# Kernel optimization log

Hardware: AMD Instinct MI355X
Metric: run time of the kernel (lower is better)

The kernel has to match this reference:

```python
import jax, jax.numpy as jnp
import numpy as np

DIM = 2048
N_HEADS = 16
HEAD_DIM = DIM // N_HEADS  # 128
HIDDEN = 8192
EPS = 1e-6
NEG = -1e9


def rmsnorm(x, w):
    xf = x.astype(jnp.float32)
    y = xf * jax.lax.rsqrt(jnp.mean(xf * xf, axis=-1, keepdims=True) + EPS)
    return y.astype(x.dtype) * w


def apply_rope(x, cos, sin):
    # x: [B,S,H,Hd]; cos/sin: [S,Hd//2] -> broadcast [1,S,1,Hd//2]
    xf = x.astype(jnp.float32)
    xr = xf[..., 0::2]
    xi = xf[..., 1::2]
    c = cos[None, :, None, :]
    s = sin[None, :, None, :]
    or_ = xr * c - xi * s
    oi_ = xr * s + xi * c
    out = jnp.stack([or_, oi_], axis=-1).reshape(x.shape)
    return out.astype(x.dtype)


def setup_inputs() -> dict:
    key = jax.random.key(0)
    ks = jax.random.split(key, 10)
    B, S = 1, 2048
    x = jax.random.normal(ks[0], (B, S, DIM), dtype=jnp.float32)
    # RoPE frequencies (Llama-style, theta=10000)
    inv_freq = 1.0 / (10000.0 ** (jnp.arange(0, HEAD_DIM, 2, dtype=jnp.float32) / HEAD_DIM))
    angles = jnp.arange(S, dtype=jnp.float32)[:, None] * inv_freq[None, :]  # [S, Hd//2]
    freqs_cos = jnp.cos(angles)
    freqs_sin = jnp.sin(angles)
    # causal additive mask [1,1,S,S]
    mask = jnp.where(jnp.tril(jnp.ones((S, S), dtype=bool)), 0.0, NEG).astype(jnp.float32)[None, None]
    sc = 0.02
    wq = jax.random.normal(ks[1], (DIM, DIM), dtype=jnp.float32) * sc
    wk = jax.random.normal(ks[2], (DIM, DIM), dtype=jnp.float32) * sc
    wv = jax.random.normal(ks[3], (DIM, DIM), dtype=jnp.float32) * sc
    wo = jax.random.normal(ks[4], (DIM, DIM), dtype=jnp.float32) * sc
    w1 = jax.random.normal(ks[5], (DIM, HIDDEN), dtype=jnp.float32) * sc
    w2 = jax.random.normal(ks[6], (HIDDEN, DIM), dtype=jnp.float32) * sc
    w3 = jax.random.normal(ks[7], (DIM, HIDDEN), dtype=jnp.float32) * sc
    attn_norm_w = jnp.ones((DIM,), dtype=jnp.float32)
    ffn_norm_w = jnp.ones((DIM,), dtype=jnp.float32)
    return {"x": x, "freqs_cos": freqs_cos, "freqs_sin": freqs_sin, "mask": mask,
            "wq": wq, "wk": wk, "wv": wv, "wo": wo, "w1": w1, "w2": w2, "w3": w3,
            "attn_norm_w": attn_norm_w, "ffn_norm_w": ffn_norm_w}


def reference(x, freqs_cos, freqs_sin, mask, wq, wk, wv, wo, w1, w2, w3, attn_norm_w, ffn_norm_w):
    B, S, D = x.shape
    # --- attention (pre-norm) ---
    hn = rmsnorm(x, attn_norm_w)
    q = (hn @ wq).reshape(B, S, N_HEADS, HEAD_DIM)
    k = (hn @ wk).reshape(B, S, N_HEADS, HEAD_DIM)
    v = (hn @ wv).reshape(B, S, N_HEADS, HEAD_DIM)
    q = apply_rope(q, freqs_cos, freqs_sin)
    k = apply_rope(k, freqs_cos, freqs_sin)
    scores = jnp.einsum('bqhd,bkhd->bhqk', q, k) / (HEAD_DIM ** 0.5) + mask
    attn = jax.nn.softmax(scores.astype(jnp.float32), axis=-1).astype(q.dtype)
    ctx = jnp.einsum('bhqk,bkhd->bqhd', attn, v).reshape(B, S, D)
    h = x + ctx @ wo
    # --- SwiGLU FFN (pre-norm) ---
    fn = rmsnorm(h, ffn_norm_w)
    ff = (jax.nn.silu(fn @ w1) * (fn @ w3)) @ w2
    return h + ff
```

## Files before the change

kernel.cpp:

```cpp
#include <hip/hip_runtime.h>
#include <hip/hip_bf16.h>

#define DIM 2048
#define HEAD_DIM 128
#define N_HEADS 16
#define SEQ 2048
#define HID 8192
#define SQKV 6144

typedef short bf16x8 __attribute__((ext_vector_type(8)));
typedef float f32x4 __attribute__((ext_vector_type(4)));
using bf16 = __hip_bfloat16;

#define MFMA16(a, b, c) __builtin_amdgcn_mfma_f32_16x16x32_bf16(a, b, c, 0, 0, 0)

__device__ __forceinline__ unsigned short f2bu(float f) {
    union { bf16 b; unsigned short u; } cv;
    cv.b = __float2bfloat16(f);
    return cv.u;
}

__device__ __forceinline__ void gl16(const void* g, void* l) {
    __builtin_amdgcn_global_load_lds(
        (const __attribute__((address_space(1))) unsigned int*)g,
        (__attribute__((address_space(3))) unsigned int*)l, 16, 0, 0);
}

__global__ __launch_bounds__(256) void rmsnorm_bf16_k(
    const float* __restrict__ x, const float* __restrict__ w, bf16* __restrict__ y)
{
    const int row = blockIdx.x;
    const int tid = threadIdx.x;
    const float* xr = x + (size_t)row * DIM;
    float4 v0 = ((const float4*)xr)[tid];
    float4 v1 = ((const float4*)xr)[tid + 256];
    float ss = v0.x*v0.x + v0.y*v0.y + v0.z*v0.z + v0.w*v0.w
             + v1.x*v1.x + v1.y*v1.y + v1.z*v1.z + v1.w*v1.w;
    for (int o = 32; o > 0; o >>= 1) ss += __shfl_down(ss, o);
    __shared__ float red[4];
    if ((tid & 63) == 0) red[tid >> 6] = ss;
    __syncthreads();
    float tot = red[0] + red[1] + red[2] + red[3];
    float r = rsqrtf(tot * (1.0f / DIM) + 1e-6f);
    float4 w0 = ((const float4*)w)[tid];
    float4 w1 = ((const float4*)w)[tid + 256];
    ushort4 o0, o1;
    o0.x = f2bu(v0.x * r * w0.x); o0.y = f2bu(v0.y * r * w0.y);
    o0.z = f2bu(v0.z * r * w0.z); o0.w = f2bu(v0.w * r * w0.w);
    o1.x = f2bu(v1.x * r * w1.x); o1.y = f2bu(v1.y * r * w1.y);
    o1.z = f2bu(v1.z * r * w1.z); o1.w = f2bu(v1.w * r * w1.w);
    ushort4* yr = (ushort4*)(y + (size_t)row * DIM);
    yr[tid] = o0;
    yr[tid + 256] = o1;
}

__global__ __launch_bounds__(256) void rmsnorm4_k(
    const float* __restrict__ part, const float* __restrict__ x,
    const float* __restrict__ w, float* __restrict__ hout, bf16* __restrict__ y)
{
    const int row = blockIdx.x;
    const int tid = threadIdx.x;
    const size_t base = (size_t)row * DIM;
    const size_t SP = (size_t)SEQ * DIM;
    float4 r0, r1;
    float ss = 0.0f;
    {
        float4 a  = ((const float4*)(x + base))[tid];
        float4 p0 = ((const float4*)(part + base))[tid];
        float4 p1 = ((const float4*)(part + SP + base))[tid];
        float4 p2 = ((const float4*)(part + 2 * SP + base))[tid];
        float4 p3 = ((const float4*)(part + 3 * SP + base))[tid];
        r0.x = a.x + ((p0.x + p1.x) + (p2.x + p3.x));
        r0.y = a.y + ((p0.y + p1.y) + (p2.y + p3.y));
        r0.z = a.z + ((p0.z + p1.z) + (p2.z + p3.z));
        r0.w = a.w + ((p0.w + p1.w) + (p2.w + p3.w));
        ((float4*)(hout + base))[tid] = r0;
        ss += r0.x*r0.x + r0.y*r0.y + r0.z*r0.z + r0.w*r0.w;
    }
    {
        const int t2 = tid + 256;
        float4 a  = ((const float4*)(x + base))[t2];
        float4 p0 = ((const float4*)(part + base))[t2];
        float4 p1 = ((const float4*)(part + SP + base))[t2];
        float4 p2 = ((const float4*)(part + 2 * SP + base))[t2];
        float4 p3 = ((const float4*)(part + 3 * SP + base))[t2];
        r1.x = a.x + ((p0.x + p1.x) + (p2.x + p3.x));
        r1.y = a.y + ((p0.y + p1.y) + (p2.y + p3.y));
        r1.z = a.z + ((p0.z + p1.z) + (p2.z + p3.z));
        r1.w = a.w + ((p0.w + p1.w) + (p2.w + p3.w));
        ((float4*)(hout + base))[t2] = r1;
        ss += r1.x*r1.x + r1.y*r1.y + r1.z*r1.z + r1.w*r1.w;
    }
    for (int o = 32; o > 0; o >>= 1) ss += __shfl_down(ss, o);
    __shared__ float red[4];
    if ((tid & 63) == 0) red[tid >> 6] = ss;
    __syncthreads();
    float tot = red[0] + red[1] + red[2] + red[3];
    float r = rsqrtf(tot * (1.0f / DIM) + 1e-6f);
    float4 w0 = ((const float4*)w)[tid];
    float4 w1 = ((const float4*)w)[tid + 256];
    ushort4 o0, o1;
    o0.x = f2bu(r0.x * r * w0.x); o0.y = f2bu(r0.y * r * w0.y);
    o0.z = f2bu(r0.z * r * w0.z); o0.w = f2bu(r0.w * r * w0.w);
    o1.x = f2bu(r1.x * r * w1.x); o1.y = f2bu(r1.y * r * w1.y);
    o1.z = f2bu(r1.z * r * w1.z); o1.w = f2bu(r1.w * r * w1.w);
    ushort4* yr = (ushort4*)(y + base);
    yr[tid] = o0;
    yr[tid + 256] = o1;
}

__global__ __launch_bounds__(256) void reduce4_k(
    const float* __restrict__ part, const float* __restrict__ h, float* __restrict__ out)
{
    const size_t i = (size_t)blockIdx.x * 256 + threadIdx.x;
    const size_t SP4 = (size_t)SEQ * DIM / 4;
    float4 a  = ((const float4*)h)[i];
    float4 p0 = ((const float4*)part)[i];
    float4 p1 = ((const float4*)part)[i + SP4];
    float4 p2 = ((const float4*)part)[i + 2 * SP4];
    float4 p3 = ((const float4*)part)[i + 3 * SP4];
    float4 r;
    r.x = a.x + ((p0.x + p1.x) + (p2.x + p3.x));
    r.y = a.y + ((p0.y + p1.y) + (p2.y + p3.y));
    r.z = a.z + ((p0.z + p1.z) + (p2.z + p3.z));
    r.w = a.w + ((p0.w + p1.w) + (p2.w + p3.w));
    ((float4*)out)[i] = r;
}

__global__ __launch_bounds__(256) void convT_f32_bf16_k(
    const float* __restrict__ in, bf16* __restrict__ out, int R, int C)
{
    __shared__ float t[32][33];
    const int tx = threadIdx.x, ty = threadIdx.y;
    const int x0 = blockIdx.x * 32, y0 = blockIdx.y * 32;
#pragma unroll
    for (int i = 0; i < 4; ++i)
        t[ty + i * 8][tx] = in[(size_t)(y0 + ty + i * 8) * C + x0 + tx];
    __syncthreads();
#pragma unroll
    for (int i = 0; i < 4; ++i)
        out[(size_t)(x0 + ty + i * 8) * R + y0 + tx] = __float2bfloat16(t[tx][ty + i * 8]);
}

__global__ __launch_bounds__(256) void convT3_f32_bf16_k(
    const float* __restrict__ wq, const float* __restrict__ wk,
    const float* __restrict__ wv, bf16* __restrict__ out)
{
    const int z = blockIdx.z;
    const float* in = z == 0 ? wq : (z == 1 ? wk : wv);
    bf16* o = out + (size_t)z * DIM * DIM;
    __shared__ float t[32][33];
    const int tx = threadIdx.x, ty = threadIdx.y;
    const int x0 = blockIdx.x * 32, y0 = blockIdx.y * 32;
#pragma unroll
    for (int i = 0; i < 4; ++i)
        t[ty + i * 8][tx] = in[(size_t)(y0 + ty + i * 8) * DIM + x0 + tx];
    __syncthreads();
#pragma unroll
    for (int i = 0; i < 4; ++i)
        o[(size_t)(x0 + ty + i * 8) * DIM + y0 + tx] = __float2bfloat16(t[tx][ty + i * 8]);
}

__global__ __launch_bounds__(256) void transpose_bf16_k(
    const bf16* __restrict__ in, int istride, bf16* __restrict__ out)
{
    __shared__ unsigned short t[32][33];
    const int tx = threadIdx.x, ty = threadIdx.y;
    const int x = blockIdx.x * 32 + tx;
    const int y0 = blockIdx.y * 32;
    const unsigned short* inu = (const unsigned short*)in;
    unsigned short* outu = (unsigned short*)out;
#pragma unroll
    for (int i = 0; i < 4; ++i)
        t[ty + i * 8][tx] = inu[(size_t)(y0 + ty + i * 8) * istride + x];
    __syncthreads();
    const int x2 = blockIdx.y * 32 + tx;
    const int y2 = blockIdx.x * 32;
#pragma unroll
    for (int i = 0; i < 4; ++i)
        outu[(size_t)(y2 + ty + i * 8) * SEQ + x2] = t[tx][ty + i * 8];
}

__global__ __launch_bounds__(256) void rope_qk_k(
    bf16* __restrict__ q, bf16* __restrict__ k,
    const float* __restrict__ cosb, const float* __restrict__ sinb)
{
    const int gid = blockIdx.x * 256 + threadIdx.x;
    const int s = gid >> 10;
    const int p = gid & 1023;
    const int h = p >> 6, j = p & 63;
    const size_t off = (size_t)s * SQKV + h * HEAD_DIM + 2 * j;
    const float c = cosb[s * 64 + j], sn = sinb[s * 64 + j];
    float xr = __bfloat162float(q[off]), xi = __bfloat162float(q[off + 1]);
    q[off]     = __float2bfloat16(xr * c - xi * sn);
    q[off + 1] = __float2bfloat16(xr * sn + xi * c);
    xr = __bfloat162float(k[off]); xi = __bfloat162float(k[off + 1]);
    k[off]     = __float2bfloat16(xr * c - xi * sn);
    k[off + 1] = __float2bfloat16(xr * sn + xi * c);
}

template <int EP>
__global__ __launch_bounds__(512, 1) void gemm256_k(
    const bf16* __restrict__ A, const bf16* __restrict__ Bt,
    bf16* __restrict__ Cb, const bf16* other, float* __restrict__ Pf,
    int M, int N, int K, int gx, int ntile, int Ks)
{
    extern __shared__ char smem[];
    const int t512 = threadIdx.x;
    const int w = t512 >> 6, lane = t512 & 63;
    const int lr = lane & 15, lg = lane >> 4;
    const int wm = w >> 2, wn = w & 3;
    const int bofs = (wn & 1) * 64;
    const int swz = (lr & 7) << 4;

    const int nwg = gridDim.x;
    const int q8 = nwg >> 3, r8 = nwg & 7;
    const int xcd = blockIdx.x & 7, seqq = blockIdx.x >> 3;
    const int wgid = (xcd < r8 ? xcd * (q8 + 1) : r8 * (q8 + 1) + (xcd - r8) * q8) + seqq;
    const int split = wgid / ntile;
    const int tile = wgid % ntile;
    const int grp = tile / (4 * gx), rem = tile % (4 * gx);
    const int m0 = (grp * 4 + (rem & 3)) * 256, n0 = (rem >> 2) * 256;
    const int kb0 = split * Ks;
    const int niter = Ks >> 7;

    const bf16* aS[2][2]; const bf16* bS[2][2];
    int sOff[2];
#pragma unroll
    for (int c = 0; c < 2; ++c) {
        const int s = (c * 512 + t512) * 16;
        const int pp = s ^ (((s >> 7) & 7) << 4);
        const int row = pp >> 7, colE = (pp & 127) >> 1;
        sOff[c] = s;
#pragma unroll
        for (int hs = 0; hs < 2; ++hs) {
            aS[hs][c] = A  + (size_t)(m0 + hs * 128 + row) * K + kb0 + colE;
            bS[hs][c] = Bt + (size_t)(n0 + hs * 128 + row) * K + kb0 + colE;
        }
    }
    auto stA = [&](int buf, int kt, int hs) {
        char* base = smem + (buf * 2 + hs) * 16384;
        gl16(aS[hs][0] + (kt << 6), base + sOff[0]);
        gl16(aS[hs][1] + (kt << 6), base + sOff[1]);
    };
    auto stB = [&](int buf, int kt, int hs) {
        char* base = smem + 65536 + (buf * 2 + hs) * 16384;
        gl16(bS[hs][0] + (kt << 6), base + sOff[0]);
        gl16(bS[hs][1] + (kt << 6), base + sOff[1]);
    };

    const char* A0m = smem + (0 * 2 + wm) * 16384;
    const char* A1m = smem + (1 * 2 + wm) * 16384;
    const char* B0m = smem + 65536 + (0 * 2 + (wn >> 1)) * 16384;
    const char* B1m = smem + 65536 + (1 * 2 + (wn >> 1)) * 16384;

    f32x4 acc[8][4] = {};
    bf16x8 bfr[4][2];
    bf16x8 x0, x1, x2, x3;

#define SBAR __builtin_amdgcn_s_barrier()
#define LGKM0 do { asm volatile("s_waitcnt lgkmcnt(0)" ::: "memory"); \
                   __builtin_amdgcn_sched_barrier(0); } while (0)
#define WVM(n) do { asm volatile("s_waitcnt vmcnt(" #n ")" ::: "memory"); \
                    __builtin_amdgcn_sched_barrier(0); } while (0)
#define LDA4(base, mf0) do { \
    x0 = *(const bf16x8*)((base) + (((mf0) * 16 + lr) * 128) + ((lg * 16) ^ swz)); \
    x1 = *(const bf16x8*)((base) + (((mf0) * 16 + lr) * 128) + ((64 + lg * 16) ^ swz)); \
    x2 = *(const bf16x8*)((base) + ((((mf0) + 1) * 16 + lr) * 128) + ((lg * 16) ^ swz)); \
    x3 = *(const bf16x8*)((base) + ((((mf0) + 1) * 16 + lr) * 128) + ((64 + lg * 16) ^ swz)); \
    } while (0)
#define LDB8(base) do { \
    _Pragma("unroll") \
    for (int nf = 0; nf < 4; ++nf) { \
        bfr[nf][0] = *(const bf16x8*)((base) + ((bofs + nf * 16 + lr) * 128) + ((lg * 16) ^ swz)); \
        bfr[nf][1] = *(const bf16x8*)((base) + ((bofs + nf * 16 + lr) * 128) + ((64 + lg * 16) ^ swz)); \
    } } while (0)
#define MFMA_PH(mf0) do { \
    _Pragma("unroll") \
    for (int nf = 0; nf < 4; ++nf) { \
        acc[(mf0)][nf]     = MFMA16(x0, bfr[nf][0], acc[(mf0)][nf]); \
        acc[(mf0)][nf]     = MFMA16(x1, bfr[nf][1], acc[(mf0)][nf]); \
        acc[(mf0) + 1][nf] = MFMA16(x2, bfr[nf][0], acc[(mf0) + 1][nf]); \
        acc[(mf0) + 1][nf] = MFMA16(x3, bfr[nf][1], acc[(mf0) + 1][nf]); \
    } } while (0)

    stB(0, 0, 0); stB(0, 0, 1); stA(0, 0, 0); stA(0, 0, 1);
    stB(1, 1, 0); stB(1, 1, 1);
    WVM(4);
    SBAR;

    for (int t = 0; t < niter; ++t) {
        const bool pf = (t + 1 < niter);
        const int k1 = 2 * t + 1, k2 = 2 * t + 2, k3 = 2 * t + 3;

        LDB8(B0m);
        LDA4(A0m, 0);
        stA(1, k1, 0);
        SBAR; LGKM0; MFMA_PH(0); SBAR;
        LDA4(A0m, 2);
        stA(1, k1, 1);
        SBAR; LGKM0; MFMA_PH(2); SBAR;
        LDA4(A0m, 4);
        if (pf) stB(0, k2, 0);
        SBAR; LGKM0; MFMA_PH(4); SBAR;
        if (pf) { WVM(2); } else { WVM(0); }
        LDA4(A0m, 6);
        if (pf) stB(0, k2, 1);
        SBAR; LGKM0; MFMA_PH(6); SBAR;
        LDB8(B1m);
        LDA4(A1m, 0);
        if (pf) stA(0, k2, 0);
        SBAR; LGKM0; MFMA_PH(0); SBAR;
        LDA4(A1m, 2);
        if (pf) stA(0, k2, 1);
        SBAR; LGKM0; MFMA_PH(2); SBAR;
        LDA4(A1m, 4);
        if (pf) stB(1, k3, 0);
        SBAR; LGKM0; MFMA_PH(4); SBAR;
        if (pf) WVM(2);
        LDA4(A1m, 6);
        if (pf) stB(1, k3, 1);
        SBAR; LGKM0; MFMA_PH(6); SBAR;
    }
#undef SBAR
#undef LGKM0
#undef WVM
#undef LDA4
#undef LDB8
#undef MFMA_PH

    float* pf_base = Pf + (size_t)split * M * N;
#pragma unroll
    for (int mf = 0; mf < 8; ++mf)
#pragma unroll
        for (int nf = 0; nf < 4; ++nf) {
            const int row = m0 + wm * 128 + mf * 16 + lg * 4;
            const int col = n0 + wn * 64 + nf * 16 + lr;
#pragma unroll
            for (int r = 0; r < 4; ++r) {
                const size_t idx = (size_t)(row + r) * N + col;
                const float v = acc[mf][nf][r];
                if (EP == 0) {
                    Cb[idx] = __float2bfloat16(v);
                } else if (EP == 2) {
                    const float gg = __bfloat162float(other[idx]);
                    const float sg = gg / (1.0f + __expf(-gg));
                    Cb[idx] = __float2bfloat16(sg * v);
                } else {
                    pf_base[idx] = v;
                }
            }
        }
}

__global__ __launch_bounds__(256) void attn_fwd_k(
    const bf16* __restrict__ qkv, const bf16* __restrict__ vT, bf16* __restrict__ ctx)
{
    const int tid = threadIdx.x;
    const int w = tid >> 6, lane = tid & 63;
    const int lr = lane & 15, lg = lane >> 4;
    const int h = blockIdx.y;
    const int qidx = (blockIdx.y < 8) ? blockIdx.x : (31 - blockIdx.x);
    const int q0b = qidx * 64;
    const int nt = qidx + 1;

    __shared__ __align__(16) unsigned short Kt[2][64 * 128];
    __shared__ __align__(16) unsigned short Vt[2][128 * 64];
    __shared__ __align__(16) unsigned short Pp[4][16 * 64];

    const char* kbase = (const char*)(qkv + DIM + h * HEAD_DIM);
    const char* vbase = (const char*)(vT + (size_t)h * HEAD_DIM * SEQ);

    const int krow_c = tid >> 4;
    const int kcolB  = (tid & 15) * 16;
    const int vrow_c = tid >> 3;
    const int vcolB  = (tid & 7) * 16;

    auto stage = [&](int buf, int kb) {
#pragma unroll
        for (int c = 0; c < 4; ++c) {
            const int r = c * 16 + krow_c;
            gl16(kbase + (size_t)(kb + r) * (SQKV * 2) + (kcolB ^ ((r & 7) << 4)),
                 &Kt[buf][c * 2048 + tid * 8]);
        }
#pragma unroll
        for (int c = 0; c < 4; ++c) {
            const int r = c * 32 + vrow_c;
            gl16(vbase + (size_t)r * (SEQ * 2) + kb * 2 + (vcolB ^ ((r & 7) << 4)),
                 &Vt[buf][c * 2048 + tid * 8]);
        }
    };

    bf16x8 qf[4];
    const bf16* qrow = qkv + (size_t)(q0b + w * 16 + lr) * SQKV + h * HEAD_DIM;
#pragma unroll
    for (int dt = 0; dt < 4; ++dt)
        qf[dt] = *(const bf16x8*)(qrow + dt * 32 + lg * 8);

    f32x4 o[8] = {};
    float m[4], l[4];
#pragma unroll
    for (int j = 0; j < 4; ++j) { m[j] = -3e38f; l[j] = 0.0f; }
    const float scale = 0.08838834764831845f;

    stage(0, 0);
    __syncthreads();

    int cur = 0;
    for (int t = 0; t < nt; ++t) {
        const int kb = t * 64;
        if (t + 1 < nt) stage(cur ^ 1, kb + 64);

        f32x4 s[4] = {};
        __builtin_amdgcn_s_setprio(1);
#pragma unroll
        for (int ss = 0; ss < 4; ++ss) {
            const int r = ss * 16 + lr;
            const int sw = (r & 7) << 3;
#pragma unroll
            for (int dt = 0; dt < 4; ++dt) {
                bf16x8 kf = *(const bf16x8*)&Kt[cur][r * 128 + ((dt * 32 + lg * 8) ^ sw)];
                s[ss] = MFMA16(qf[dt], kf, s[ss]);
            }
        }
        __builtin_amdgcn_s_setprio(0);

        float al[4];
#pragma unroll
        for (int j = 0; j < 4; ++j) {
            const int qi = q0b + w * 16 + lg * 4 + j;
            const int prow = lg * 4 + j;
            const int psw = (prow & 7) << 3;
            float a[4];
#pragma unroll
            for (int ss = 0; ss < 4; ++ss)
                a[ss] = s[ss][j] * scale + ((kb + ss * 16 + lr) > qi ? -1e9f : 0.0f);
            float mx = fmaxf(fmaxf(a[0], a[1]), fmaxf(a[2], a[3]));
            mx = fmaxf(mx, __shfl_xor(mx, 1));
            mx = fmaxf(mx, __shfl_xor(mx, 2));
            mx = fmaxf(mx, __shfl_xor(mx, 4));
            mx = fmaxf(mx, __shfl_xor(mx, 8));
            const float mn = fmaxf(m[j], mx);
            const float asc = __expf(m[j] - mn);
            float e0 = __expf(a[0] - mn), e1 = __expf(a[1] - mn);
            float e2 = __expf(a[2] - mn), e3 = __expf(a[3] - mn);
            float rs = (e0 + e1) + (e2 + e3);
            rs += __shfl_xor(rs, 1); rs += __shfl_xor(rs, 2);
            rs += __shfl_xor(rs, 4); rs += __shfl_xor(rs, 8);
            l[j] = l[j] * asc + rs;
            m[j] = mn;
            al[j] = asc;
            Pp[w][prow * 64 + ((lr)      ^ psw)] = f2bu(e0);
            Pp[w][prow * 64 + ((16 + lr) ^ psw)] = f2bu(e1);
            Pp[w][prow * 64 + ((32 + lr) ^ psw)] = f2bu(e2);
            Pp[w][prow * 64 + ((48 + lr) ^ psw)] = f2bu(e3);
        }
#pragma unroll
        for (int d2 = 0; d2 < 8; ++d2)
#pragma unroll
            for (int j = 0; j < 4; ++j) o[d2][j] *= al[j];

        asm volatile("s_waitcnt lgkmcnt(0)" ::: "memory");
        __builtin_amdgcn_sched_barrier(0);
        const int asw = (lr & 7) << 3;
        bf16x8 pa0 = *(const bf16x8*)&Pp[w][lr * 64 + ((lg * 8)      ^ asw)];
        bf16x8 pa1 = *(const bf16x8*)&Pp[w][lr * 64 + ((32 + lg * 8) ^ asw)];

        __builtin_amdgcn_s_setprio(1);
#pragma unroll
        for (int d2 = 0; d2 < 8; ++d2) {
            const int rv = d2 * 16 + lr;
            const int vsw = (rv & 7) << 3;
            bf16x8 vf0 = *(const bf16x8*)&Vt[cur][rv * 64 + ((lg * 8)      ^ vsw)];
            bf16x8 vf1 = *(const bf16x8*)&Vt[cur][rv * 64 + ((32 + lg * 8) ^ vsw)];
            o[d2] = MFMA16(pa0, vf0, o[d2]);
            o[d2] = MFMA16(pa1, vf1, o[d2]);
        }
        __builtin_amdgcn_s_setprio(0);

        __syncthreads();
        cur ^= 1;
    }

#pragma unroll
    for (int j = 0; j < 4; ++j) {
        const float inv = 1.0f / l[j];
        bf16* dst = ctx + (size_t)(q0b + w * 16 + lg * 4 + j) * DIM + h * HEAD_DIM + lr;
#pragma unroll
        for (int d2 = 0; d2 < 8; ++d2)
            dst[d2 * 16] = __float2bfloat16(o[d2][j] * inv);
    }
}

extern "C" void kernel_launch(void* const* d_in, const int* in_sizes, int n_in,
                              void* d_out, int out_size, void* d_ws, size_t ws_size,
                              hipStream_t stream)
{
    const float* x   = (const float*)d_in[0];
    const float* fc  = (const float*)d_in[1];
    const float* fs  = (const float*)d_in[2];
    const float* wq  = (const float*)d_in[4];
    const float* wk  = (const float*)d_in[5];
    const float* wv  = (const float*)d_in[6];
    const float* wo  = (const float*)d_in[7];
    const float* w1  = (const float*)d_in[8];
    const float* w2  = (const float*)d_in[9];
    const float* w3  = (const float*)d_in[10];
    const float* anw = (const float*)d_in[11];
    const float* fnw = (const float*)d_in[12];
    float* out = (float*)d_out;

    char* p = (char*)d_ws;
    auto alloc = [&](size_t n) { char* r = p; p += (n + 255) & ~(size_t)255; return r; };
    bf16* wT  = (bf16*)alloc((size_t)HID * DIM * 2);
    bf16* hn  = (bf16*)alloc((size_t)SEQ * DIM * 2);
    bf16* qkv = (bf16*)alloc((size_t)SEQ * SQKV * 2);
    bf16* vt  = (bf16*)alloc((size_t)SEQ * DIM * 2);
    bf16* ctx = (bf16*)alloc((size_t)SEQ * DIM * 2);
    bf16* fn  = (bf16*)alloc((size_t)SEQ * DIM * 2);
    float* h  = (float*)alloc((size_t)SEQ * DIM * 4);
    bf16* g   = (bf16*)alloc((size_t)SEQ * HID * 2);
    float* sk = (float*)alloc((size_t)4 * SEQ * DIM * 4);

    const dim3 tb32(32, 8);
    const int LDS256 = 131072;
    (void)hipFuncSetAttribute((const void*)gemm256_k<0>,
        hipFuncAttributeMaxDynamicSharedMemorySize, LDS256);
    (void)hipFuncSetAttribute((const void*)gemm256_k<2>,
        hipFuncAttributeMaxDynamicSharedMemorySize, LDS256);
    (void)hipFuncSetAttribute((const void*)gemm256_k<3>,
        hipFuncAttributeMaxDynamicSharedMemorySize, LDS256);

    rmsnorm_bf16_k<<<SEQ, 256, 0, stream>>>(x, anw, hn);

    convT3_f32_bf16_k<<<dim3(DIM / 32, DIM / 32, 3), tb32, 0, stream>>>(wq, wk, wv, wT);
    gemm256_k<0><<<(SEQ / 256) * (SQKV / 256), 512, LDS256, stream>>>(
        hn, wT, qkv, nullptr, nullptr, SEQ, SQKV, DIM, SQKV / 256, (SEQ / 256) * (SQKV / 256), DIM);

    rope_qk_k<<<(SEQ * 1024) / 256, 256, 0, stream>>>(qkv, qkv + DIM, fc, fs);
    transpose_bf16_k<<<dim3(DIM / 32, SEQ / 32), tb32, 0, stream>>>(qkv + 2 * DIM, SQKV, vt);

    attn_fwd_k<<<dim3(SEQ / 64, N_HEADS), 256, 0, stream>>>(qkv, vt, ctx);

    convT_f32_bf16_k<<<dim3(DIM / 32, DIM / 32), tb32, 0, stream>>>(wo, wT, DIM, DIM);
    gemm256_k<3><<<(SEQ / 256) * (DIM / 256) * 4, 512, LDS256, stream>>>(
        ctx, wT, nullptr, nullptr, sk, SEQ, DIM, DIM, DIM / 256, (SEQ / 256) * (DIM / 256), 512);
    rmsnorm4_k<<<SEQ, 256, 0, stream>>>(sk, x, fnw, h, fn);

    convT_f32_bf16_k<<<dim3(HID / 32, DIM / 32), tb32, 0, stream>>>(w1, wT, DIM, HID);
    gemm256_k<0><<<(SEQ / 256) * (HID / 256), 512, LDS256, stream>>>(
        fn, wT, g, nullptr, nullptr, SEQ, HID, DIM, HID / 256, (SEQ / 256) * (HID / 256), DIM);
    convT_f32_bf16_k<<<dim3(HID / 32, DIM / 32), tb32, 0, stream>>>(w3, wT, DIM, HID);
    gemm256_k<2><<<(SEQ / 256) * (HID / 256), 512, LDS256, stream>>>(
        fn, wT, g, g, nullptr, SEQ, HID, DIM, HID / 256, (SEQ / 256) * (HID / 256), DIM);

    convT_f32_bf16_k<<<dim3(DIM / 32, HID / 32), tb32, 0, stream>>>(w2, wT, HID, DIM);
    gemm256_k<3><<<(SEQ / 256) * (DIM / 256) * 4, 512, LDS256, stream>>>(
        g, wT, nullptr, nullptr, sk, SEQ, DIM, HID, DIM / 256, (SEQ / 256) * (DIM / 256), 2048);
    reduce4_k<<<(SEQ * DIM / 4) / 256, 256, 0, stream>>>(sk, h, out);
}
```

Before: 510.3 us.

## Fuse w1 and w3 FFN GEMMs with interleaved weights and in-epilogue SwiGLU

The separate w1 and w3 GEMMs are replaced by one GEMM over a combined B matrix of 2*HID columns. B rows are interleaved in 16-row groups from the w1 and w3 transposes, so each wave holds matching gate and up accumulators and computes silu(a)*b in the epilogue. This removes the intermediate write and re-read of the gate tensor and one kernel launch. The w3 transpose reuses the dead hn/qkv workspace region. MFMA phases are also wrapped in s_setprio to favour the math waves during scheduling.

```diff
diff --git a/kernel.cpp b/kernel.cpp
--- a/kernel.cpp
+++ b/kernel.cpp
@@ -201,8 +201,8 @@
 
 template <int EP>
 __global__ __launch_bounds__(512, 1) void gemm256_k(
-    const bf16* __restrict__ A, const bf16* __restrict__ Bt,
-    bf16* __restrict__ Cb, const bf16* other, float* __restrict__ Pf,
+    const bf16* __restrict__ A, const bf16* __restrict__ Bt, const bf16* __restrict__ Bt2,
+    bf16* __restrict__ Cb, float* __restrict__ Pf,
     int M, int N, int K, int gx, int ntile, int Ks)
 {
     extern __shared__ char smem[];
@@ -234,8 +234,16 @@
         sOff[c] = s;
 #pragma unroll
         for (int hs = 0; hs < 2; ++hs) {
-            aS[hs][c] = A  + (size_t)(m0 + hs * 128 + row) * K + kb0 + colE;
-            bS[hs][c] = Bt + (size_t)(n0 + hs * 128 + row) * K + kb0 + colE;
+            aS[hs][c] = A + (size_t)(m0 + hs * 128 + row) * K + kb0 + colE;
+            const int rg = n0 + hs * 128 + row;
+            if (EP == 4) {
+                const int g = rg >> 4;
+                const bf16* src = (g & 1) ? Bt2 : Bt;
+                const int j = ((g >> 1) << 4) + (rg & 15);
+                bS[hs][c] = src + (size_t)j * K + kb0 + colE;
+            } else {
+                bS[hs][c] = Bt + (size_t)rg * K + kb0 + colE;
+            }
         }
     }
     auto stA = [&](int buf, int kt, int hs) {
@@ -276,13 +284,15 @@
         bfr[nf][1] = *(const bf16x8*)((base) + ((bofs + nf * 16 + lr) * 128) + ((64 + lg * 16) ^ swz)); \
     } } while (0)
 #define MFMA_PH(mf0) do { \
+    __builtin_amdgcn_s_setprio(1); \
     _Pragma("unroll") \
     for (int nf = 0; nf < 4; ++nf) { \
         acc[(mf0)][nf]     = MFMA16(x0, bfr[nf][0], acc[(mf0)][nf]); \
         acc[(mf0)][nf]     = MFMA16(x1, bfr[nf][1], acc[(mf0)][nf]); \
         acc[(mf0) + 1][nf] = MFMA16(x2, bfr[nf][0], acc[(mf0) + 1][nf]); \
         acc[(mf0) + 1][nf] = MFMA16(x3, bfr[nf][1], acc[(mf0) + 1][nf]); \
-    } } while (0)
+    } \
+    __builtin_amdgcn_s_setprio(0); } while (0)
 
     stB(0, 0, 0); stB(0, 0, 1); stA(0, 0, 0); stA(0, 0, 1);
     stB(1, 1, 0); stB(1, 1, 1);
@@ -329,28 +339,40 @@
 #undef LDB8
 #undef MFMA_PH
 
-    float* pf_base = Pf + (size_t)split * M * N;
-#pragma unroll
-    for (int mf = 0; mf < 8; ++mf)
-#pragma unroll
-        for (int nf = 0; nf < 4; ++nf) {
-            const int row = m0 + wm * 128 + mf * 16 + lg * 4;
-            const int col = n0 + wn * 64 + nf * 16 + lr;
-#pragma unroll
-            for (int r = 0; r < 4; ++r) {
-                const size_t idx = (size_t)(row + r) * N + col;
-                const float v = acc[mf][nf][r];
-                if (EP == 0) {
-                    Cb[idx] = __float2bfloat16(v);
-                } else if (EP == 2) {
-                    const float gg = __bfloat162float(other[idx]);
-                    const float sg = gg / (1.0f + __expf(-gg));
-                    Cb[idx] = __float2bfloat16(sg * v);
-                } else {
-                    pf_base[idx] = v;
+    if (EP == 4) {
+        const int jb = (n0 >> 1) + wn * 32;
+        const int NH = N >> 1;
+#pragma unroll
+        for (int mf = 0; mf < 8; ++mf)
+#pragma unroll
+            for (int pp = 0; pp < 4; pp += 2) {
+                const int row = m0 + wm * 128 + mf * 16 + lg * 4;
+                const int j = jb + (pp >> 1) * 16 + lr;
+#pragma unroll
+                for (int r = 0; r < 4; ++r) {
+                    const float a = acc[mf][pp][r];
+                    const float b = acc[mf][pp + 1][r];
+                    const float s = a / (1.0f + __expf(-a));
+                    Cb[(size_t)(row + r) * NH + j] = __float2bfloat16(s * b);
                 }
             }
-        }
+    } else {
+        float* pf_base = Pf + (size_t)split * M * N;
+#pragma unroll
+        for (int mf = 0; mf < 8; ++mf)
+#pragma unroll
+            for (int nf = 0; nf < 4; ++nf) {
+                const int row = m0 + wm * 128 + mf * 16 + lg * 4;
+                const int col = n0 + wn * 64 + nf * 16 + lr;
+#pragma unroll
+                for (int r = 0; r < 4; ++r) {
+                    const size_t idx = (size_t)(row + r) * N + col;
+                    const float v = acc[mf][nf][r];
+                    if (EP == 0) Cb[idx] = __float2bfloat16(v);
+                    else         pf_base[idx] = v;
+                }
+            }
+    }
 }
 
 __global__ __launch_bounds__(256) void attn_fwd_k(
@@ -521,21 +543,22 @@
     float* h  = (float*)alloc((size_t)SEQ * DIM * 4);
     bf16* g   = (bf16*)alloc((size_t)SEQ * HID * 2);
     float* sk = (float*)alloc((size_t)4 * SEQ * DIM * 4);
+    bf16* w3T = hn;
 
     const dim3 tb32(32, 8);
     const int LDS256 = 131072;
     (void)hipFuncSetAttribute((const void*)gemm256_k<0>,
         hipFuncAttributeMaxDynamicSharedMemorySize, LDS256);
-    (void)hipFuncSetAttribute((const void*)gemm256_k<2>,
-        hipFuncAttributeMaxDynamicSharedMemorySize, LDS256);
     (void)hipFuncSetAttribute((const void*)gemm256_k<3>,
         hipFuncAttributeMaxDynamicSharedMemorySize, LDS256);
+    (void)hipFuncSetAttribute((const void*)gemm256_k<4>,
+        hipFuncAttributeMaxDynamicSharedMemorySize, LDS256);
 
     rmsnorm_bf16_k<<<SEQ, 256, 0, stream>>>(x, anw, hn);
 
     convT3_f32_bf16_k<<<dim3(DIM / 32, DIM / 32, 3), tb32, 0, stream>>>(wq, wk, wv, wT);
     gemm256_k<0><<<(SEQ / 256) * (SQKV / 256), 512, LDS256, stream>>>(
-        hn, wT, qkv, nullptr, nullptr, SEQ, SQKV, DIM, SQKV / 256, (SEQ / 256) * (SQKV / 256), DIM);
+        hn, wT, nullptr, qkv, nullptr, SEQ, SQKV, DIM, SQKV / 256, (SEQ / 256) * (SQKV / 256), DIM);
 
     rope_qk_k<<<(SEQ * 1024) / 256, 256, 0, stream>>>(qkv, qkv + DIM, fc, fs);
     transpose_bf16_k<<<dim3(DIM / 32, SEQ / 32), tb32, 0, stream>>>(qkv + 2 * DIM, SQKV, vt);
@@ -548,11 +571,10 @@
     rmsnorm4_k<<<SEQ, 256, 0, stream>>>(sk, x, fnw, h, fn);
 
     convT_f32_bf16_k<<<dim3(HID / 32, DIM / 32), tb32, 0, stream>>>(w1, wT, DIM, HID);
-    gemm256_k<0><<<(SEQ / 256) * (HID / 256), 512, LDS256, stream>>>(
-        fn, wT, g, nullptr, nullptr, SEQ, HID, DIM, HID / 256, (SEQ / 256) * (HID / 256), DIM);
-    convT_f32_bf16_k<<<dim3(HID / 32, DIM / 32), tb32, 0, stream>>>(w3, wT, DIM, HID);
-    gemm256_k<2><<<(SEQ / 256) * (HID / 256), 512, LDS256, stream>>>(
-        fn, wT, g, g, nullptr, SEQ, HID, DIM, HID / 256, (SEQ / 256) * (HID / 256), DIM);
+    convT_f32_bf16_k<<<dim3(HID / 32, DIM / 32), tb32, 0, stream>>>(w3, w3T, DIM, HID);
+    gemm256_k<4><<<(SEQ / 256) * ((2 * HID) / 256), 512, LDS256, stream>>>(
+        fn, wT, w3T, g, nullptr, SEQ, 2 * HID, DIM, (2 * HID) / 256,
+        (SEQ / 256) * ((2 * HID) / 256), DIM);
 
     convT_f32_bf16_k<<<dim3(DIM / 32, HID / 32), tb32, 0, stream>>>(w2, wT, HID, DIM);
     gemm256_k<3><<<(SEQ / 256) * (DIM / 256) * 4, 512, LDS256, stream>>>(
```

Result: faster. 491.4 us (-3.7%).
